# Performance work log

Hardware: AMD Instinct MI355X
Metric: run time of the kernel (lower is better)

The kernel has to match this reference:

```python
import jax, jax.numpy as jnp
import numpy as np


def setup_inputs() -> dict:
    key = jax.random.key(0)
    B, I, H = 8192, 1024, 1024
    C = I + H
    ks = jax.random.split(key, 7)
    # Xavier-uniform bound for Linear(C, H)
    bound = float(np.sqrt(6.0 / (C + H)))
    def xavier(k):
        return jax.random.uniform(k, (H, C), jnp.float32, -bound, bound)
    return {
        "x": jax.random.normal(ks[0], (B, I), jnp.float32),
        "h": jax.random.normal(ks[1], (B, H), jnp.float32),
        "c": jax.random.normal(ks[2], (B, H), jnp.float32),
        "W_i": xavier(ks[3]),
        "W_f": xavier(ks[4]),
        "W_o": xavier(ks[5]),
        "W_g": xavier(ks[6]),
        "b_i": jnp.zeros((H,), jnp.float32),
        "b_f": jnp.zeros((H,), jnp.float32),
        "b_o": jnp.zeros((H,), jnp.float32),
        "b_g": jnp.zeros((H,), jnp.float32),
    }


def reference(x, h, c, W_i, W_f, W_o, W_g, b_i, b_f, b_o, b_g):
    # combined: [B, input+hidden]
    combined = jnp.concatenate([x, h], axis=1)
    # fuse 4 gate GEMMs into one: W stacked -> [4H, C]
    W = jnp.concatenate([W_i, W_f, W_o, W_g], axis=0)
    b = jnp.concatenate([b_i, b_f, b_o, b_g], axis=0)
    gates = combined @ W.T + b  # [B, 4H]
    i_pre, f_pre, o_pre, g_pre = jnp.split(gates, 4, axis=1)
    i = jax.nn.sigmoid(i_pre)
    f = jax.nn.sigmoid(f_pre)
    o = jax.nn.sigmoid(o_pre)
    g = jnp.tanh(g_pre)
    c_t = f * c + i * g
    h_t = o * jnp.tanh(c_t)
    return (h_t, c_t)
```

## Files before the change

### kernel.cpp

```cpp
#include <hip/hip_runtime.h>
#include <hip/hip_bf16.h>
#include <stdint.h>


typedef __bf16 bf16x8 __attribute__((ext_vector_type(8)));
typedef float f32x4 __attribute__((ext_vector_type(4)));

#define B_DIM 8192
#define H_DIM 1024
#define C_DIM 2048

#define XH_ELEMS (B_DIM * H_DIM)
#define W_ELEMS  (H_DIM * C_DIM)
#define CVT_TOTAL (2 * XH_ELEMS + 4 * W_ELEMS)
#define WS_NEEDED ((size_t)CVT_TOTAL * 2)

__device__ __forceinline__ void async_cp16(void* lds_dst, const void* g_src) {
    __builtin_amdgcn_global_load_lds(
        (const __attribute__((address_space(1))) void*)g_src,
        (__attribute__((address_space(3))) void*)lds_dst,
        16, 0, 0);
}

__device__ __forceinline__ bf16x8 lds_read16(const void* p) {
    bf16x8 r;
    asm volatile("ds_read_b128 %0, %1"
                 : "=v"(r)
                 : "v"((const __attribute__((address_space(3))) void*)p));
    return r;
}

__global__ __launch_bounds__(256)
void cvt_kernel(const float* __restrict__ x, const float* __restrict__ h,
                const float* __restrict__ wi, const float* __restrict__ wf,
                const float* __restrict__ wo, const float* __restrict__ wg,
                __hip_bfloat16* __restrict__ dst)
{
    const size_t stride = (size_t)gridDim.x * 256;
    for (size_t t = (size_t)blockIdx.x * 256 + threadIdx.x;
         t < (size_t)(CVT_TOTAL / 8); t += stride) {
        const size_t base = t * 8;
        const float* src;
        size_t off;
        if (base < (size_t)XH_ELEMS)            { src = x; off = base; }
        else if (base < (size_t)2 * XH_ELEMS)   { src = h; off = base - XH_ELEMS; }
        else {
            const size_t wb = base - (size_t)2 * XH_ELEMS;
            const int g = (int)(wb >> 21);
            off = wb & (size_t)(W_ELEMS - 1);
            src = (g == 0) ? wi : (g == 1) ? wf : (g == 2) ? wo : wg;
        }
        const f32x4 v0 = *(const f32x4*)(src + off);
        const f32x4 v1 = *(const f32x4*)(src + off + 4);
        __hip_bfloat16 tmp[8];
        tmp[0] = __float2bfloat16(v0[0]); tmp[1] = __float2bfloat16(v0[1]);
        tmp[2] = __float2bfloat16(v0[2]); tmp[3] = __float2bfloat16(v0[3]);
        tmp[4] = __float2bfloat16(v1[0]); tmp[5] = __float2bfloat16(v1[1]);
        tmp[6] = __float2bfloat16(v1[2]); tmp[7] = __float2bfloat16(v1[3]);
        *(bf16x8*)(dst + base) = *(const bf16x8*)tmp;
    }
}

__global__ __launch_bounds__(512, 2)
void lstm_gemm_bf16(const __hip_bfloat16* __restrict__ xb,
                    const __hip_bfloat16* __restrict__ hb,
                    const __hip_bfloat16* __restrict__ Wb,
                    const float* __restrict__ c,
                    const float* __restrict__ pbi, const float* __restrict__ pbf,
                    const float* __restrict__ pbo, const float* __restrict__ pbg,
                    float* __restrict__ out)
{
    __shared__ __hip_bfloat16 lds[2][2][256][64];
    char* const ldsBase = (char*)&lds[0][0][0][0];

    const int tid  = threadIdx.x;
    const int lane = tid & 63;
    const int wave = tid >> 6;
    const int wr   = wave >> 2;
    const int wc   = wave & 3;
    const int quad = lane >> 4;
    const int l16  = lane & 15;

    const int bid = (int)blockIdx.x;
    const int swz = (bid & 7) * 64 + (bid >> 3);
    const int m_base = (swz >> 4) * 256;
    const int n0     = (swz & 15) * 64;

    uint32_t aOff[2][2], bOff[2][2];
#pragma unroll
    for (int a = 0; a < 2; ++a) {
        const int li  = a * 512 + tid;
        const int row = li >> 3;
        const int sch = ((li & 7) ^ (row & 7)) * 8;
#pragma unroll
        for (int hh = 0; hh < 2; ++hh) {
            aOff[hh][a] = (uint32_t)(m_base + hh * 128 + row) * H_DIM + (uint32_t)sch;
            const int g   = (hh << 1) | ((row >> 4) & 1);
            const int hco = ((row >> 5) << 4) | (row & 15);
            bOff[hh][a] = (uint32_t)g * (uint32_t)W_ELEMS
                        + (uint32_t)(n0 + hco) * (uint32_t)C_DIM + (uint32_t)sch;
        }
    }
    const uint32_t dstT = (uint32_t)tid * 16u;

#define STAGE_A(pO, hh, srcp, kel) do {                                                        \
    async_cp16(ldsBase + (pO) + (hh) * 16384u + 0u    + dstT, (srcp) + aOff[hh][0] + (kel));   \
    async_cp16(ldsBase + (pO) + (hh) * 16384u + 8192u + dstT, (srcp) + aOff[hh][1] + (kel));   \
} while (0)
#define STAGE_B(pO, hh, kel) do {                                                              \
    async_cp16(ldsBase + (pO) + 32768u + (hh) * 16384u + 0u    + dstT, Wb + bOff[hh][0] + (kel)); \
    async_cp16(ldsBase + (pO) + 32768u + (hh) * 16384u + 8192u + dstT, Wb + bOff[hh][1] + (kel)); \
} while (0)

    const uint32_t cb    = (uint32_t)((quad ^ (l16 & 7)) * 16);
    const uint32_t aBase = (uint32_t)(wr * 64 + l16) * 128u + cb;
    const uint32_t bBase = 32768u + (uint32_t)(wc * 32 + l16) * 128u + cb;

#define LDA(dstv, pO, ihh, ii, ss) \
    dstv = lds_read16(ldsBase + (pO) + ((aBase + (ihh) * 16384u + (ii) * 2048u) ^ ((uint32_t)(ss) << 6)))
#define LDB(dstv, pO, jj, ss) \
    dstv = lds_read16(ldsBase + (pO) + ((bBase + (((jj) >> 1)) * 16384u + ((jj) & 1) * 2048u) ^ ((uint32_t)(ss) << 6)))

    f32x4 acc[8][4];
#pragma unroll
    for (int i = 0; i < 8; ++i)
#pragma unroll
        for (int j = 0; j < 4; ++j)
            acc[i][j] = (f32x4){0.f, 0.f, 0.f, 0.f};

    STAGE_A(0u, 0, xb, 0u);
    STAGE_B(0u, 0, 0u);
    STAGE_B(0u, 1, 0u);
    STAGE_A(0u, 1, xb, 0u);
    STAGE_A(65536u, 0, xb, 64u);
    STAGE_B(65536u, 0, 64u);
    STAGE_B(65536u, 1, 64u);
    asm volatile("s_waitcnt vmcnt(6)" ::: "memory");
    __builtin_amdgcn_s_barrier();

    bf16x8 av0[4][2], av1[4][2], bv0[2][2], bv1[2][2];
#pragma unroll
    for (int i = 0; i < 4; ++i) { LDA(av0[i][0], 0u, 0, i, 0); LDA(av0[i][1], 0u, 0, i, 1); }
    LDB(bv0[0][0], 0u, 0, 0); LDB(bv0[1][0], 0u, 1, 0);
    LDB(bv0[0][1], 0u, 0, 1); LDB(bv0[1][1], 0u, 1, 1);

#define MFMA_Q(AV, BV, IOFF, JOFF) do {                                                   \
    _Pragma("unroll")                                                                     \
    for (int i = 0; i < 4; ++i)                                                           \
        _Pragma("unroll")                                                                 \
        for (int j = 0; j < 2; ++j)                                                       \
            acc[i + (IOFF)][j + (JOFF)] = __builtin_amdgcn_mfma_f32_16x16x32_bf16(        \
                AV[i][0], BV[j][0], acc[i + (IOFF)][j + (JOFF)], 0, 0, 0);                \
    _Pragma("unroll")                                                                     \
    for (int i = 0; i < 4; ++i)                                                           \
        _Pragma("unroll")                                                                 \
        for (int j = 0; j < 2; ++j)                                                       \
            acc[i + (IOFF)][j + (JOFF)] = __builtin_amdgcn_mfma_f32_16x16x32_bf16(        \
                AV[i][1], BV[j][1], acc[i + (IOFF)][j + (JOFF)], 0, 0, 0);                \
} while (0)

    for (int u = 0; u < 31; ++u) {
        const uint32_t pO = (uint32_t)(u & 1) * 65536u;
        const uint32_t qO = pO ^ 65536u;
        const __hip_bfloat16* aS1 = (u + 1 < 16) ? xb : hb;
        const uint32_t ak1 = (uint32_t)((u + 1) & 15) * 64u;
        const __hip_bfloat16* aS2 = (u + 2 < 16) ? xb : hb;
        const uint32_t ak2 = (uint32_t)((u + 2) & 15) * 64u;
        const uint32_t bk2 = (uint32_t)(u + 2) * 64u;

        LDB(bv1[0][0], pO, 2, 0); LDB(bv1[1][0], pO, 3, 0);
        LDB(bv1[0][1], pO, 2, 1); LDB(bv1[1][1], pO, 3, 1);
        STAGE_A(qO, 1, aS1, ak1);
        __builtin_amdgcn_s_barrier();
        asm volatile("s_waitcnt lgkmcnt(4)" ::: "memory");
        __builtin_amdgcn_sched_barrier(0);
        __builtin_amdgcn_s_setprio(1);
        MFMA_Q(av0, bv0, 0, 0);
        __builtin_amdgcn_s_setprio(0);
        __builtin_amdgcn_s_barrier();

#pragma unroll
        for (int i = 0; i < 4; ++i) { LDA(av1[i][0], pO, 1, i, 0); LDA(av1[i][1], pO, 1, i, 1); }
        if (u < 30) STAGE_A(pO, 0, aS2, ak2);
        __builtin_amdgcn_s_barrier();
        asm volatile("s_waitcnt lgkmcnt(8)" ::: "memory");
        __builtin_amdgcn_sched_barrier(0);
        __builtin_amdgcn_s_setprio(1);
        MFMA_Q(av0, bv1, 0, 2);
        __builtin_amdgcn_s_setprio(0);
        if (u < 30)  { asm volatile("s_waitcnt vmcnt(2)" ::: "memory"); }
        else         { asm volatile("s_waitcnt vmcnt(0)" ::: "memory"); }
        __builtin_amdgcn_s_barrier();

#pragma unroll
        for (int i = 0; i < 4; ++i) { LDA(av0[i][0], qO, 0, i, 0); LDA(av0[i][1], qO, 0, i, 1); }
        if (u < 30) STAGE_B(pO, 0, bk2);
        __builtin_amdgcn_s_barrier();
        asm volatile("s_waitcnt lgkmcnt(8)" ::: "memory");
        __builtin_amdgcn_sched_barrier(0);
        __builtin_amdgcn_s_setprio(1);
        MFMA_Q(av1, bv0, 4, 0);
        __builtin_amdgcn_s_setprio(0);
        __builtin_amdgcn_s_barrier();

        LDB(bv0[0][0], qO, 0, 0); LDB(bv0[1][0], qO, 1, 0);
        LDB(bv0[0][1], qO, 0, 1); LDB(bv0[1][1], qO, 1, 1);
        if (u < 30) STAGE_B(pO, 1, bk2);
        __builtin_amdgcn_s_barrier();
        asm volatile("s_waitcnt lgkmcnt(12)" ::: "memory");
        __builtin_amdgcn_sched_barrier(0);
        __builtin_amdgcn_s_setprio(1);
        MFMA_Q(av1, bv1, 4, 2);
        __builtin_amdgcn_s_setprio(0);
        __builtin_amdgcn_s_barrier();
    }

    {
        const uint32_t pO = 65536u;
        LDB(bv1[0][0], pO, 2, 0); LDB(bv1[1][0], pO, 3, 0);
        LDB(bv1[0][1], pO, 2, 1); LDB(bv1[1][1], pO, 3, 1);
        __builtin_amdgcn_s_barrier();
        asm volatile("s_waitcnt lgkmcnt(4)" ::: "memory");
        __builtin_amdgcn_sched_barrier(0);
        MFMA_Q(av0, bv0, 0, 0);
        __builtin_amdgcn_s_barrier();
#pragma unroll
        for (int i = 0; i < 4; ++i) { LDA(av1[i][0], pO, 1, i, 0); LDA(av1[i][1], pO, 1, i, 1); }
        __builtin_amdgcn_s_barrier();
        asm volatile("s_waitcnt lgkmcnt(8)" ::: "memory");
        __builtin_amdgcn_sched_barrier(0);
        MFMA_Q(av0, bv1, 0, 2);
        __builtin_amdgcn_s_barrier();
        asm volatile("s_waitcnt lgkmcnt(0)" ::: "memory");
        __builtin_amdgcn_sched_barrier(0);
        MFMA_Q(av1, bv0, 4, 0);
        MFMA_Q(av1, bv1, 4, 2);
    }

#undef MFMA_Q
#undef STAGE_A
#undef STAGE_B
#undef LDA
#undef LDB

    const int col = n0 + wc * 16 + l16;
    const float vbi = pbi[col];
    const float vbf = pbf[col];
    const float vbo = pbo[col];
    const float vbg = pbg[col];
    const size_t HB = (size_t)B_DIM * H_DIM;
#pragma unroll
    for (int i = 0; i < 8; ++i) {
        const int fb  = (i < 4) ? (wr * 64 + i * 16) : (128 + wr * 64 + (i - 4) * 16);
        const int mb0 = m_base + fb + quad * 4;
#pragma unroll
        for (int r = 0; r < 4; ++r) {
            const size_t m = (size_t)(mb0 + r);
            const float ip = acc[i][0][r] + vbi;
            const float fp = acc[i][1][r] + vbf;
            const float op = acc[i][2][r] + vbo;
            const float gp = acc[i][3][r] + vbg;
            const float ig = 1.f / (1.f + __expf(-ip));
            const float fg = 1.f / (1.f + __expf(-fp));
            const float og = 1.f / (1.f + __expf(-op));
            const float eg = __expf(-2.f * fabsf(gp));
            const float gg = copysignf((1.f - eg) / (1.f + eg), gp);
            const float cin = c[m * H_DIM + col];
            const float ct = fg * cin + ig * gg;
            const float ec = __expf(-2.f * fabsf(ct));
            const float tc = copysignf((1.f - ec) / (1.f + ec), ct);
            out[m * H_DIM + col]      = og * tc;
            out[HB + m * H_DIM + col] = ct;
        }
    }
}

#define BM 128
#define BNC 32
#define BK 64
#define K_ITERS (C_DIM / BK)

__global__ __launch_bounds__(256, 2)
void lstm_gemm_fused(const float* __restrict__ x, const float* __restrict__ h,
                     const float* __restrict__ Wi, const float* __restrict__ Wf,
                     const float* __restrict__ Wo, const float* __restrict__ Wg,
                     const float* __restrict__ c,
                     const float* __restrict__ pbi, const float* __restrict__ pbf,
                     const float* __restrict__ pbo, const float* __restrict__ pbg,
                     float* __restrict__ out)
{
    __shared__ __hip_bfloat16 As[BM][BK];
    __shared__ __hip_bfloat16 Bs[BM][BK];

    const int tid  = threadIdx.x;
    const int lane = tid & 63;
    const int wave = tid >> 6;
    const int wr   = wave >> 1;
    const int wc   = wave & 1;
    const int quad = lane >> 4;
    const int l16  = lane & 15;

    const int m_base = blockIdx.y * BM;
    const int n0     = blockIdx.x * BNC;

    const int srow = tid >> 1;
    const int scol = (tid & 1) * 32;
    const float* aS[2] = {
        x + (size_t)(m_base + srow) * H_DIM + scol,
        h + (size_t)(m_base + srow) * H_DIM + scol
    };
    const int gate = (srow >> 4) & 3;
    const int grow = n0 + ((srow >> 6) << 4) + (srow & 15);
    const float* Wsel = (gate == 0) ? Wi : (gate == 1) ? Wf : (gate == 2) ? Wo : Wg;
    const float* bS = Wsel + (size_t)grow * C_DIM + scol;

    int aRow[4], bRow[4];
#pragma unroll
    for (int i = 0; i < 4; ++i) aRow[i] = wr * 64 + i * 16 + l16;
#pragma unroll
    for (int j = 0; j < 4; ++j) bRow[j] = wc * 64 + j * 16 + l16;

    f32x4 acc[4][4];
#pragma unroll
    for (int i = 0; i < 4; ++i)
#pragma unroll
        for (int j = 0; j < 4; ++j)
            acc[i][j] = (f32x4){0.f, 0.f, 0.f, 0.f};

    for (int kt = 0; kt < K_ITERS; ++kt) {
        const int hsel = (kt >= (H_DIM / BK));
        const int koff = (kt & ((H_DIM / BK) - 1)) * BK;
        const float* ap = aS[hsel] + koff;
        const float* bp = bS + kt * BK;
        __hip_bfloat16 ta[32], tb[32];
#pragma unroll
        for (int q = 0; q < 8; ++q) {
            f32x4 a = *(const f32x4*)(ap + q * 4);
            f32x4 b = *(const f32x4*)(bp + q * 4);
            ta[q*4+0]=__float2bfloat16(a[0]); ta[q*4+1]=__float2bfloat16(a[1]);
            ta[q*4+2]=__float2bfloat16(a[2]); ta[q*4+3]=__float2bfloat16(a[3]);
            tb[q*4+0]=__float2bfloat16(b[0]); tb[q*4+1]=__float2bfloat16(b[1]);
            tb[q*4+2]=__float2bfloat16(b[2]); tb[q*4+3]=__float2bfloat16(b[3]);
        }
#pragma unroll
        for (int q = 0; q < 4; ++q) {
            const int ch  = (scol / 8) + q;
            const int sl  = ch ^ (srow & 7);
            *(bf16x8*)((char*)&As[0][0] + srow * (BK * 2) + sl * 16) = *(const bf16x8*)&ta[q * 8];
            *(bf16x8*)((char*)&Bs[0][0] + srow * (BK * 2) + sl * 16) = *(const bf16x8*)&tb[q * 8];
        }
        __syncthreads();

#pragma unroll
        for (int s = 0; s < 2; ++s) {
            bf16x8 av[4], bv[4];
#pragma unroll
            for (int i = 0; i < 4; ++i) {
                const int r  = aRow[i];
                const int ch = (s * 4 + quad) ^ (r & 7);
                av[i] = *(const bf16x8*)((const char*)&As[0][0] + r * (BK * 2) + ch * 16);
            }
#pragma unroll
            for (int j = 0; j < 4; ++j) {
                const int r  = bRow[j];
                const int ch = (s * 4 + quad) ^ (r & 7);
                bv[j] = *(const bf16x8*)((const char*)&Bs[0][0] + r * (BK * 2) + ch * 16);
            }
#pragma unroll
            for (int i = 0; i < 4; ++i)
#pragma unroll
                for (int j = 0; j < 4; ++j)
                    acc[i][j] = __builtin_amdgcn_mfma_f32_16x16x32_bf16(
                        av[i], bv[j], acc[i][j], 0, 0, 0);
        }
        __syncthreads();
    }

    const int col = n0 + wc * 16 + l16;
    const float vbi = pbi[col];
    const float vbf = pbf[col];
    const float vbo = pbo[col];
    const float vbg = pbg[col];
    const size_t HB = (size_t)B_DIM * H_DIM;
#pragma unroll
    for (int i = 0; i < 4; ++i) {
        const int mb = m_base + wr * 64 + i * 16 + quad * 4;
#pragma unroll
        for (int r = 0; r < 4; ++r) {
            const size_t m = (size_t)(mb + r);
            const float ip = acc[i][0][r] + vbi;
            const float fp = acc[i][1][r] + vbf;
            const float op = acc[i][2][r] + vbo;
            const float gp = acc[i][3][r] + vbg;
            const float ig = 1.f / (1.f + __expf(-ip));
            const float fg = 1.f / (1.f + __expf(-fp));
            const float og = 1.f / (1.f + __expf(-op));
            const float eg = __expf(-2.f * fabsf(gp));
            const float gg = copysignf((1.f - eg) / (1.f + eg), gp);
            const float cin = c[m * H_DIM + col];
            const float ct = fg * cin + ig * gg;
            const float ec = __expf(-2.f * fabsf(ct));
            const float tc = copysignf((1.f - ec) / (1.f + ec), ct);
            out[m * H_DIM + col]      = og * tc;
            out[HB + m * H_DIM + col] = ct;
        }
    }
}

extern "C" void kernel_launch(void* const* d_in, const int* in_sizes, int n_in,
                              void* d_out, int out_size, void* d_ws, size_t ws_size,
                              hipStream_t stream) {
    const float* x  = (const float*)d_in[0];
    const float* h  = (const float*)d_in[1];
    const float* c  = (const float*)d_in[2];
    const float* Wi = (const float*)d_in[3];
    const float* Wf = (const float*)d_in[4];
    const float* Wo = (const float*)d_in[5];
    const float* Wg = (const float*)d_in[6];
    const float* bi = (const float*)d_in[7];
    const float* bfp= (const float*)d_in[8];
    const float* bo = (const float*)d_in[9];
    const float* bg = (const float*)d_in[10];
    float* out = (float*)d_out;

    if (ws_size >= WS_NEEDED) {
        __hip_bfloat16* wsb = (__hip_bfloat16*)d_ws;
        cvt_kernel<<<2048, 256, 0, stream>>>(x, h, Wi, Wf, Wo, Wg, wsb);
        lstm_gemm_bf16<<<512, 512, 0, stream>>>(
            wsb, wsb + XH_ELEMS, wsb + 2 * (size_t)XH_ELEMS,
            c, bi, bfp, bo, bg, out);
    } else {
        lstm_gemm_fused<<<dim3(H_DIM / BNC, B_DIM / BM), dim3(256), 0, stream>>>(
            x, h, Wi, Wf, Wo, Wg, c, bi, bfp, bo, bg, out);
    }
}
```

Measured before the change: 307.5 us.

## Fuse fp32-to-bf16 conversion into the pipelined GEMM, dropping the separate convert pass

Removes the separate conversion kernel that wrote bf16 copies of x, h and the four weight matrices to workspace. The 256x64-tile GEMM now loads fp32 directly from global memory into registers, converts to bf16 and writes to LDS, staged across the four MFMA quarters of each k-step. This avoids a full extra read/write pass over the activations and weights. In exchange, the async global-to-LDS copies become synchronous register loads with more VGPR pressure, fp32 global traffic inside the GEMM doubles, and the per-tile conversion is repeated across blocks.

Measured after the change: 336.6 us. 1.09x slower.

```diff
diff --git a/kernel.cpp b/kernel.cpp
--- a/kernel.cpp
+++ b/kernel.cpp
@@ -9,18 +9,7 @@
 #define B_DIM 8192
 #define H_DIM 1024
 #define C_DIM 2048
-
-#define XH_ELEMS (B_DIM * H_DIM)
-#define W_ELEMS  (H_DIM * C_DIM)
-#define CVT_TOTAL (2 * XH_ELEMS + 4 * W_ELEMS)
-#define WS_NEEDED ((size_t)CVT_TOTAL * 2)
-
-__device__ __forceinline__ void async_cp16(void* lds_dst, const void* g_src) {
-    __builtin_amdgcn_global_load_lds(
-        (const __attribute__((address_space(1))) void*)g_src,
-        (__attribute__((address_space(3))) void*)lds_dst,
-        16, 0, 0);
-}
+#define W_ELEMS (H_DIM * C_DIM)
 
 __device__ __forceinline__ bf16x8 lds_read16(const void* p) {
     bf16x8 r;
@@ -30,45 +19,14 @@
     return r;
 }
 
-__global__ __launch_bounds__(256)
-void cvt_kernel(const float* __restrict__ x, const float* __restrict__ h,
-                const float* __restrict__ wi, const float* __restrict__ wf,
-                const float* __restrict__ wo, const float* __restrict__ wg,
-                __hip_bfloat16* __restrict__ dst)
-{
-    const size_t stride = (size_t)gridDim.x * 256;
-    for (size_t t = (size_t)blockIdx.x * 256 + threadIdx.x;
-         t < (size_t)(CVT_TOTAL / 8); t += stride) {
-        const size_t base = t * 8;
-        const float* src;
-        size_t off;
-        if (base < (size_t)XH_ELEMS)            { src = x; off = base; }
-        else if (base < (size_t)2 * XH_ELEMS)   { src = h; off = base - XH_ELEMS; }
-        else {
-            const size_t wb = base - (size_t)2 * XH_ELEMS;
-            const int g = (int)(wb >> 21);
-            off = wb & (size_t)(W_ELEMS - 1);
-            src = (g == 0) ? wi : (g == 1) ? wf : (g == 2) ? wo : wg;
-        }
-        const f32x4 v0 = *(const f32x4*)(src + off);
-        const f32x4 v1 = *(const f32x4*)(src + off + 4);
-        __hip_bfloat16 tmp[8];
-        tmp[0] = __float2bfloat16(v0[0]); tmp[1] = __float2bfloat16(v0[1]);
-        tmp[2] = __float2bfloat16(v0[2]); tmp[3] = __float2bfloat16(v0[3]);
-        tmp[4] = __float2bfloat16(v1[0]); tmp[5] = __float2bfloat16(v1[1]);
-        tmp[6] = __float2bfloat16(v1[2]); tmp[7] = __float2bfloat16(v1[3]);
-        *(bf16x8*)(dst + base) = *(const bf16x8*)tmp;
-    }
-}
-
 __global__ __launch_bounds__(512, 2)
-void lstm_gemm_bf16(const __hip_bfloat16* __restrict__ xb,
-                    const __hip_bfloat16* __restrict__ hb,
-                    const __hip_bfloat16* __restrict__ Wb,
-                    const float* __restrict__ c,
-                    const float* __restrict__ pbi, const float* __restrict__ pbf,
-                    const float* __restrict__ pbo, const float* __restrict__ pbg,
-                    float* __restrict__ out)
+void lstm_fused256(const float* __restrict__ x, const float* __restrict__ h,
+                   const float* __restrict__ Wi, const float* __restrict__ Wf,
+                   const float* __restrict__ Wo, const float* __restrict__ Wg,
+                   const float* __restrict__ c,
+                   const float* __restrict__ pbi, const float* __restrict__ pbf,
+                   const float* __restrict__ pbo, const float* __restrict__ pbg,
+                   float* __restrict__ out)
 {
     __shared__ __hip_bfloat16 lds[2][2][256][64];
     char* const ldsBase = (char*)&lds[0][0][0][0];
@@ -86,31 +44,51 @@
     const int m_base = (swz >> 4) * 256;
     const int n0     = (swz & 15) * 64;
 
-    uint32_t aOff[2][2], bOff[2][2];
+    uint32_t aOffF[2][2];
+    const float* Wp[2][2];
+    uint32_t dstOff[2];
 #pragma unroll
     for (int a = 0; a < 2; ++a) {
         const int li  = a * 512 + tid;
         const int row = li >> 3;
         const int sch = ((li & 7) ^ (row & 7)) * 8;
+        dstOff[a] = (uint32_t)li * 16u;
 #pragma unroll
         for (int hh = 0; hh < 2; ++hh) {
-            aOff[hh][a] = (uint32_t)(m_base + hh * 128 + row) * H_DIM + (uint32_t)sch;
+            aOffF[hh][a] = (uint32_t)(m_base + hh * 128 + row) * H_DIM + (uint32_t)sch;
             const int g   = (hh << 1) | ((row >> 4) & 1);
             const int hco = ((row >> 5) << 4) | (row & 15);
-            bOff[hh][a] = (uint32_t)g * (uint32_t)W_ELEMS
-                        + (uint32_t)(n0 + hco) * (uint32_t)C_DIM + (uint32_t)sch;
+            const float* Wsel = (g == 0) ? Wi : (g == 1) ? Wf : (g == 2) ? Wo : Wg;
+            Wp[hh][a] = Wsel + (size_t)(n0 + hco) * C_DIM + sch;
         }
     }
-    const uint32_t dstT = (uint32_t)tid * 16u;
-
-#define STAGE_A(pO, hh, srcp, kel) do {                                                        \
-    async_cp16(ldsBase + (pO) + (hh) * 16384u + 0u    + dstT, (srcp) + aOff[hh][0] + (kel));   \
-    async_cp16(ldsBase + (pO) + (hh) * 16384u + 8192u + dstT, (srcp) + aOff[hh][1] + (kel));   \
-} while (0)
-#define STAGE_B(pO, hh, kel) do {                                                              \
-    async_cp16(ldsBase + (pO) + 32768u + (hh) * 16384u + 0u    + dstT, Wb + bOff[hh][0] + (kel)); \
-    async_cp16(ldsBase + (pO) + 32768u + (hh) * 16384u + 8192u + dstT, Wb + bOff[hh][1] + (kel)); \
-} while (0)
+
+    f32x4 rA[4], rB[4];
+
+#define LOAD_A(REG, hh, SRC, KEL) do {                                              \
+    _Pragma("unroll")                                                               \
+    for (int a_ = 0; a_ < 2; ++a_) {                                                \
+        REG[a_ * 2]     = *(const f32x4*)((SRC) + aOffF[hh][a_] + (KEL));           \
+        REG[a_ * 2 + 1] = *(const f32x4*)((SRC) + aOffF[hh][a_] + (KEL) + 4);       \
+    } } while (0)
+#define LOAD_B(REG, hh, KEL) do {                                                   \
+    _Pragma("unroll")                                                               \
+    for (int a_ = 0; a_ < 2; ++a_) {                                                \
+        REG[a_ * 2]     = *(const f32x4*)(Wp[hh][a_] + (KEL));                      \
+        REG[a_ * 2 + 1] = *(const f32x4*)(Wp[hh][a_] + (KEL) + 4);                  \
+    } } while (0)
+#define WRITE_HALF(REG, BUFO, REGION) do {                                          \
+    _Pragma("unroll")                                                               \
+    for (int a_ = 0; a_ < 2; ++a_) {                                                \
+        __hip_bfloat16 t_[8];                                                       \
+        t_[0] = __float2bfloat16(REG[a_*2][0]);  t_[1] = __float2bfloat16(REG[a_*2][1]); \
+        t_[2] = __float2bfloat16(REG[a_*2][2]);  t_[3] = __float2bfloat16(REG[a_*2][3]); \
+        t_[4] = __float2bfloat16(REG[a_*2+1][0]); t_[5] = __float2bfloat16(REG[a_*2+1][1]); \
+        t_[6] = __float2bfloat16(REG[a_*2+1][2]); t_[7] = __float2bfloat16(REG[a_*2+1][3]); \
+        *(bf16x8*)(ldsBase + (BUFO) + (REGION) + dstOff[a_]) = *(const bf16x8*)t_;  \
+    } } while (0)
+#define WRITE_A(REG, BUFO, hh) WRITE_HALF(REG, BUFO, (uint32_t)(hh) * 16384u)
+#define WRITE_B(REG, BUFO, hh) WRITE_HALF(REG, BUFO, 32768u + (uint32_t)(hh) * 16384u)
 
     const uint32_t cb    = (uint32_t)((quad ^ (l16 & 7)) * 16);
     const uint32_t aBase = (uint32_t)(wr * 64 + l16) * 128u + cb;
@@ -120,29 +98,6 @@
     dstv = lds_read16(ldsBase + (pO) + ((aBase + (ihh) * 16384u + (ii) * 2048u) ^ ((uint32_t)(ss) << 6)))
 #define LDB(dstv, pO, jj, ss) \
     dstv = lds_read16(ldsBase + (pO) + ((bBase + (((jj) >> 1)) * 16384u + ((jj) & 1) * 2048u) ^ ((uint32_t)(ss) << 6)))
-
-    f32x4 acc[8][4];
-#pragma unroll
-    for (int i = 0; i < 8; ++i)
-#pragma unroll
-        for (int j = 0; j < 4; ++j)
-            acc[i][j] = (f32x4){0.f, 0.f, 0.f, 0.f};
-
-    STAGE_A(0u, 0, xb, 0u);
-    STAGE_B(0u, 0, 0u);
-    STAGE_B(0u, 1, 0u);
-    STAGE_A(0u, 1, xb, 0u);
-    STAGE_A(65536u, 0, xb, 64u);
-    STAGE_B(65536u, 0, 64u);
-    STAGE_B(65536u, 1, 64u);
-    asm volatile("s_waitcnt vmcnt(6)" ::: "memory");
-    __builtin_amdgcn_s_barrier();
-
-    bf16x8 av0[4][2], av1[4][2], bv0[2][2], bv1[2][2];
-#pragma unroll
-    for (int i = 0; i < 4; ++i) { LDA(av0[i][0], 0u, 0, i, 0); LDA(av0[i][1], 0u, 0, i, 1); }
-    LDB(bv0[0][0], 0u, 0, 0); LDB(bv0[1][0], 0u, 1, 0);
-    LDB(bv0[0][1], 0u, 0, 1); LDB(bv0[1][1], 0u, 1, 1);
 
 #define MFMA_Q(AV, BV, IOFF, JOFF) do {                                                   \
     _Pragma("unroll")                                                                     \
@@ -159,89 +114,90 @@
                 AV[i][1], BV[j][1], acc[i + (IOFF)][j + (JOFF)], 0, 0, 0);                \
 } while (0)
 
-    for (int u = 0; u < 31; ++u) {
+    f32x4 acc[8][4];
+#pragma unroll
+    for (int i = 0; i < 8; ++i)
+#pragma unroll
+        for (int j = 0; j < 4; ++j)
+            acc[i][j] = (f32x4){0.f, 0.f, 0.f, 0.f};
+
+    LOAD_A(rA, 0, x, 0u);
+    LOAD_B(rB, 0, 0u);
+    WRITE_A(rA, 0u, 0);  LOAD_A(rA, 1, x, 0u);
+    WRITE_B(rB, 0u, 0);  LOAD_B(rB, 1, 0u);
+    WRITE_A(rA, 0u, 1);  LOAD_A(rA, 0, x, 64u);
+    WRITE_B(rB, 0u, 1);  LOAD_B(rB, 0, 64u);
+    WRITE_A(rA, 65536u, 0);
+    WRITE_B(rB, 65536u, 0);
+    LOAD_B(rA, 1, 64u);
+    asm volatile("s_waitcnt lgkmcnt(0)" ::: "memory");
+    __builtin_amdgcn_s_barrier();
+
+    bf16x8 av[4][2], bv0[2][2], bv1[2][2];
+
+    for (int u = 0; u < 32; ++u) {
         const uint32_t pO = (uint32_t)(u & 1) * 65536u;
         const uint32_t qO = pO ^ 65536u;
-        const __hip_bfloat16* aS1 = (u + 1 < 16) ? xb : hb;
+        const float* aS1 = (u + 1 < 16) ? x : h;
         const uint32_t ak1 = (uint32_t)((u + 1) & 15) * 64u;
-        const __hip_bfloat16* aS2 = (u + 2 < 16) ? xb : hb;
+        const float* aS2 = (u + 2 < 16) ? x : h;
         const uint32_t ak2 = (uint32_t)((u + 2) & 15) * 64u;
         const uint32_t bk2 = (uint32_t)(u + 2) * 64u;
 
+#pragma unroll
+        for (int i = 0; i < 4; ++i) { LDA(av[i][0], pO, 0, i, 0); LDA(av[i][1], pO, 0, i, 1); }
+        LDB(bv0[0][0], pO, 0, 0); LDB(bv0[1][0], pO, 1, 0);
+        LDB(bv0[0][1], pO, 0, 1); LDB(bv0[1][1], pO, 1, 1);
+        if (u < 31) { LOAD_A(rB, 1, aS1, ak1); WRITE_B(rA, qO, 1); }
+        __builtin_amdgcn_s_barrier();
+        asm volatile("s_waitcnt lgkmcnt(0)" ::: "memory");
+        __builtin_amdgcn_sched_barrier(0);
+        __builtin_amdgcn_s_setprio(1);
+        MFMA_Q(av, bv0, 0, 0);
+        __builtin_amdgcn_s_setprio(0);
+        __builtin_amdgcn_s_barrier();
+
         LDB(bv1[0][0], pO, 2, 0); LDB(bv1[1][0], pO, 3, 0);
         LDB(bv1[0][1], pO, 2, 1); LDB(bv1[1][1], pO, 3, 1);
-        STAGE_A(qO, 1, aS1, ak1);
-        __builtin_amdgcn_s_barrier();
-        asm volatile("s_waitcnt lgkmcnt(4)" ::: "memory");
-        __builtin_amdgcn_sched_barrier(0);
-        __builtin_amdgcn_s_setprio(1);
-        MFMA_Q(av0, bv0, 0, 0);
-        __builtin_amdgcn_s_setprio(0);
-        __builtin_amdgcn_s_barrier();
-
-#pragma unroll
-        for (int i = 0; i < 4; ++i) { LDA(av1[i][0], pO, 1, i, 0); LDA(av1[i][1], pO, 1, i, 1); }
-        if (u < 30) STAGE_A(pO, 0, aS2, ak2);
-        __builtin_amdgcn_s_barrier();
-        asm volatile("s_waitcnt lgkmcnt(8)" ::: "memory");
-        __builtin_amdgcn_sched_barrier(0);
-        __builtin_amdgcn_s_setprio(1);
-        MFMA_Q(av0, bv1, 0, 2);
-        __builtin_amdgcn_s_setprio(0);
-        if (u < 30)  { asm volatile("s_waitcnt vmcnt(2)" ::: "memory"); }
-        else         { asm volatile("s_waitcnt vmcnt(0)" ::: "memory"); }
-        __builtin_amdgcn_s_barrier();
-
-#pragma unroll
-        for (int i = 0; i < 4; ++i) { LDA(av0[i][0], qO, 0, i, 0); LDA(av0[i][1], qO, 0, i, 1); }
-        if (u < 30) STAGE_B(pO, 0, bk2);
-        __builtin_amdgcn_s_barrier();
-        asm volatile("s_waitcnt lgkmcnt(8)" ::: "memory");
-        __builtin_amdgcn_sched_barrier(0);
-        __builtin_amdgcn_s_setprio(1);
-        MFMA_Q(av1, bv0, 4, 0);
-        __builtin_amdgcn_s_setprio(0);
-        __builtin_amdgcn_s_barrier();
-
-        LDB(bv0[0][0], qO, 0, 0); LDB(bv0[1][0], qO, 1, 0);
-        LDB(bv0[0][1], qO, 0, 1); LDB(bv0[1][1], qO, 1, 1);
-        if (u < 30) STAGE_B(pO, 1, bk2);
-        __builtin_amdgcn_s_barrier();
-        asm volatile("s_waitcnt lgkmcnt(12)" ::: "memory");
-        __builtin_amdgcn_sched_barrier(0);
-        __builtin_amdgcn_s_setprio(1);
-        MFMA_Q(av1, bv1, 4, 2);
+        if (u < 30) LOAD_A(rA, 0, aS2, ak2);
+        if (u < 31) WRITE_A(rB, qO, 1);
+        __builtin_amdgcn_s_barrier();
+        asm volatile("s_waitcnt lgkmcnt(0)" ::: "memory");
+        __builtin_amdgcn_sched_barrier(0);
+        __builtin_amdgcn_s_setprio(1);
+        MFMA_Q(av, bv1, 0, 2);
+        __builtin_amdgcn_s_setprio(0);
+        __builtin_amdgcn_s_barrier();
+
+#pragma unroll
+        for (int i = 0; i < 4; ++i) { LDA(av[i][0], pO, 1, i, 0); LDA(av[i][1], pO, 1, i, 1); }
+        if (u < 30) { LOAD_B(rB, 0, bk2); WRITE_A(rA, pO, 0); }
+        __builtin_amdgcn_s_barrier();
+        asm volatile("s_waitcnt lgkmcnt(0)" ::: "memory");
+        __builtin_amdgcn_sched_barrier(0);
+        __builtin_amdgcn_s_setprio(1);
+        MFMA_Q(av, bv0, 4, 0);
+        __builtin_amdgcn_s_setprio(0);
+        __builtin_amdgcn_s_barrier();
+
+        if (u < 30) { LOAD_B(rA, 1, bk2); WRITE_B(rB, pO, 0); }
+        __builtin_amdgcn_s_barrier();
+        asm volatile("s_waitcnt lgkmcnt(0)" ::: "memory");
+        __builtin_amdgcn_sched_barrier(0);
+        __builtin_amdgcn_s_setprio(1);
+        MFMA_Q(av, bv1, 4, 2);
         __builtin_amdgcn_s_setprio(0);
         __builtin_amdgcn_s_barrier();
     }
 
-    {
-        const uint32_t pO = 65536u;
-        LDB(bv1[0][0], pO, 2, 0); LDB(bv1[1][0], pO, 3, 0);
-        LDB(bv1[0][1], pO, 2, 1); LDB(bv1[1][1], pO, 3, 1);
-        __builtin_amdgcn_s_barrier();
-        asm volatile("s_waitcnt lgkmcnt(4)" ::: "memory");
-        __builtin_amdgcn_sched_barrier(0);
-        MFMA_Q(av0, bv0, 0, 0);
-        __builtin_amdgcn_s_barrier();
-#pragma unroll
-        for (int i = 0; i < 4; ++i) { LDA(av1[i][0], pO, 1, i, 0); LDA(av1[i][1], pO, 1, i, 1); }
-        __builtin_amdgcn_s_barrier();
-        asm volatile("s_waitcnt lgkmcnt(8)" ::: "memory");
-        __builtin_amdgcn_sched_barrier(0);
-        MFMA_Q(av0, bv1, 0, 2);
-        __builtin_amdgcn_s_barrier();
-        asm volatile("s_waitcnt lgkmcnt(0)" ::: "memory");
-        __builtin_amdgcn_sched_barrier(0);
-        MFMA_Q(av1, bv0, 4, 0);
-        MFMA_Q(av1, bv1, 4, 2);
-    }
-
-#undef MFMA_Q
-#undef STAGE_A
-#undef STAGE_B
+#undef LOAD_A
+#undef LOAD_B
+#undef WRITE_HALF
+#undef WRITE_A
+#undef WRITE_B
 #undef LDA
 #undef LDB
+#undef MFMA_Q
 
     const int col = n0 + wc * 16 + l16;
     const float vbi = pbi[col];
@@ -275,138 +231,6 @@
     }
 }
 
-#define BM 128
-#define BNC 32
-#define BK 64
-#define K_ITERS (C_DIM / BK)
-
-__global__ __launch_bounds__(256, 2)
-void lstm_gemm_fused(const float* __restrict__ x, const float* __restrict__ h,
-                     const float* __restrict__ Wi, const float* __restrict__ Wf,
-                     const float* __restrict__ Wo, const float* __restrict__ Wg,
-                     const float* __restrict__ c,
-                     const float* __restrict__ pbi, const float* __restrict__ pbf,
-                     const float* __restrict__ pbo, const float* __restrict__ pbg,
-                     float* __restrict__ out)
-{
-    __shared__ __hip_bfloat16 As[BM][BK];
-    __shared__ __hip_bfloat16 Bs[BM][BK];
-
-    const int tid  = threadIdx.x;
-    const int lane = tid & 63;
-    const int wave = tid >> 6;
-    const int wr   = wave >> 1;
-    const int wc   = wave & 1;
-    const int quad = lane >> 4;
-    const int l16  = lane & 15;
-
-    const int m_base = blockIdx.y * BM;
-    const int n0     = blockIdx.x * BNC;
-
-    const int srow = tid >> 1;
-    const int scol = (tid & 1) * 32;
-    const float* aS[2] = {
-        x + (size_t)(m_base + srow) * H_DIM + scol,
-        h + (size_t)(m_base + srow) * H_DIM + scol
-    };
-    const int gate = (srow >> 4) & 3;
-    const int grow = n0 + ((srow >> 6) << 4) + (srow & 15);
-    const float* Wsel = (gate == 0) ? Wi : (gate == 1) ? Wf : (gate == 2) ? Wo : Wg;
-    const float* bS = Wsel + (size_t)grow * C_DIM + scol;
-
-    int aRow[4], bRow[4];
-#pragma unroll
-    for (int i = 0; i < 4; ++i) aRow[i] = wr * 64 + i * 16 + l16;
-#pragma unroll
-    for (int j = 0; j < 4; ++j) bRow[j] = wc * 64 + j * 16 + l16;
-
-    f32x4 acc[4][4];
-#pragma unroll
-    for (int i = 0; i < 4; ++i)
-#pragma unroll
-        for (int j = 0; j < 4; ++j)
-            acc[i][j] = (f32x4){0.f, 0.f, 0.f, 0.f};
-
-    for (int kt = 0; kt < K_ITERS; ++kt) {
-        const int hsel = (kt >= (H_DIM / BK));
-        const int koff = (kt & ((H_DIM / BK) - 1)) * BK;
-        const float* ap = aS[hsel] + koff;
-        const float* bp = bS + kt * BK;
-        __hip_bfloat16 ta[32], tb[32];
-#pragma unroll
-        for (int q = 0; q < 8; ++q) {
-            f32x4 a = *(const f32x4*)(ap + q * 4);
-            f32x4 b = *(const f32x4*)(bp + q * 4);
-            ta[q*4+0]=__float2bfloat16(a[0]); ta[q*4+1]=__float2bfloat16(a[1]);
-            ta[q*4+2]=__float2bfloat16(a[2]); ta[q*4+3]=__float2bfloat16(a[3]);
-            tb[q*4+0]=__float2bfloat16(b[0]); tb[q*4+1]=__float2bfloat16(b[1]);
-            tb[q*4+2]=__float2bfloat16(b[2]); tb[q*4+3]=__float2bfloat16(b[3]);
-        }
-#pragma unroll
-        for (int q = 0; q < 4; ++q) {
-            const int ch  = (scol / 8) + q;
-            const int sl  = ch ^ (srow & 7);
-            *(bf16x8*)((char*)&As[0][0] + srow * (BK * 2) + sl * 16) = *(const bf16x8*)&ta[q * 8];
-            *(bf16x8*)((char*)&Bs[0][0] + srow * (BK * 2) + sl * 16) = *(const bf16x8*)&tb[q * 8];
-        }
-        __syncthreads();
-
-#pragma unroll
-        for (int s = 0; s < 2; ++s) {
-            bf16x8 av[4], bv[4];
-#pragma unroll
-            for (int i = 0; i < 4; ++i) {
-                const int r  = aRow[i];
-                const int ch = (s * 4 + quad) ^ (r & 7);
-                av[i] = *(const bf16x8*)((const char*)&As[0][0] + r * (BK * 2) + ch * 16);
-            }
-#pragma unroll
-            for (int j = 0; j < 4; ++j) {
-                const int r  = bRow[j];
-                const int ch = (s * 4 + quad) ^ (r & 7);
-                bv[j] = *(const bf16x8*)((const char*)&Bs[0][0] + r * (BK * 2) + ch * 16);
-            }
-#pragma unroll
-            for (int i = 0; i < 4; ++i)
-#pragma unroll
-                for (int j = 0; j < 4; ++j)
-                    acc[i][j] = __builtin_amdgcn_mfma_f32_16x16x32_bf16(
-                        av[i], bv[j], acc[i][j], 0, 0, 0);
-        }
-        __syncthreads();
-    }
-
-    const int col = n0 + wc * 16 + l16;
-    const float vbi = pbi[col];
-    const float vbf = pbf[col];
-    const float vbo = pbo[col];
-    const float vbg = pbg[col];
-    const size_t HB = (size_t)B_DIM * H_DIM;
-#pragma unroll
-    for (int i = 0; i < 4; ++i) {
-        const int mb = m_base + wr * 64 + i * 16 + quad * 4;
-#pragma unroll
-        for (int r = 0; r < 4; ++r) {
-            const size_t m = (size_t)(mb + r);
-            const float ip = acc[i][0][r] + vbi;
-            const float fp = acc[i][1][r] + vbf;
-            const float op = acc[i][2][r] + vbo;
-            const float gp = acc[i][3][r] + vbg;
-            const float ig = 1.f / (1.f + __expf(-ip));
-            const float fg = 1.f / (1.f + __expf(-fp));
-            const float og = 1.f / (1.f + __expf(-op));
-            const float eg = __expf(-2.f * fabsf(gp));
-            const float gg = copysignf((1.f - eg) / (1.f + eg), gp);
-            const float cin = c[m * H_DIM + col];
-            const float ct = fg * cin + ig * gg;
-            const float ec = __expf(-2.f * fabsf(ct));
-            const float tc = copysignf((1.f - ec) / (1.f + ec), ct);
-            out[m * H_DIM + col]      = og * tc;
-            out[HB + m * H_DIM + col] = ct;
-        }
-    }
-}
-
 extern "C" void kernel_launch(void* const* d_in, const int* in_sizes, int n_in,
                               void* d_out, int out_size, void* d_ws, size_t ws_size,
                               hipStream_t stream) {
@@ -422,15 +246,8 @@
     const float* bo = (const float*)d_in[9];
     const float* bg = (const float*)d_in[10];
     float* out = (float*)d_out;
-
-    if (ws_size >= WS_NEEDED) {
-        __hip_bfloat16* wsb = (__hip_bfloat16*)d_ws;
-        cvt_kernel<<<2048, 256, 0, stream>>>(x, h, Wi, Wf, Wo, Wg, wsb);
-        lstm_gemm_bf16<<<512, 512, 0, stream>>>(
-            wsb, wsb + XH_ELEMS, wsb + 2 * (size_t)XH_ELEMS,
-            c, bi, bfp, bo, bg, out);
-    } else {
-        lstm_gemm_fused<<<dim3(H_DIM / BNC, B_DIM / BM), dim3(256), 0, stream>>>(
-            x, h, Wi, Wf, Wo, Wg, c, bi, bfp, bo, bg, out);
-    }
+    (void)d_ws; (void)ws_size;
+
+    lstm_fused256<<<512, 512, 0, stream>>>(
+        x, h, Wi, Wf, Wo, Wg, c, bi, bfp, bo, bg, out);
 }
```
